# Kernel optimization log

Hardware: AMD Instinct MI355X
Metric: run time of the kernel (lower is better)

Reference implementation:

```python
import jax, jax.numpy as jnp
import numpy as np

N, E, B = 10000, 160000, 64
ND, ED, H, L, C = 128, 64, 256, 4, 10
LN_EPS = 1e-5


def _layernorm(x, g, b):
    mu = jnp.mean(x, axis=-1, keepdims=True)
    var = jnp.mean(jnp.square(x - mu), axis=-1, keepdims=True)
    return (x - mu) * jax.lax.rsqrt(var + LN_EPS) * g + b


def setup_inputs() -> dict:
    key = jax.random.key(0)
    ks = jax.random.split(key, 24)

    def w(k, shape, fan_in):
        return jax.random.normal(k, shape, jnp.float32) * (1.0 / np.sqrt(fan_in))

    node_features = jax.random.normal(ks[0], (N, ND), jnp.float32)
    edge_index = jax.random.randint(ks[1], (2, E), 0, N, jnp.int64)
    edge_features = jax.random.normal(ks[2], (E, ED), jnp.float32)
    # deterministic sorted batch assignment (no empty graphs)
    batch = (jnp.arange(N, dtype=jnp.int64) * B) // N

    inp = dict(
        node_features=node_features,
        edge_index=edge_index,
        edge_features=edge_features,
        batch=batch,
        node_W=w(ks[3], (ND, H), ND), node_b=jnp.zeros((H,), jnp.float32),
        edge_W=w(ks[4], (ED, H), ED), edge_b=jnp.zeros((H,), jnp.float32),
        msg_W1=w(ks[5], (L, 3 * H, H), 3 * H), msg_b1=jnp.zeros((L, H), jnp.float32),
        msg_W2=w(ks[6], (L, H, H), H), msg_b2=jnp.zeros((L, H), jnp.float32),
        upd_W1=w(ks[7], (L, 2 * H, H), 2 * H), upd_b1=jnp.zeros((L, H), jnp.float32),
        upd_W2=w(ks[8], (L, H, H), H), upd_b2=jnp.zeros((L, H), jnp.float32),
        ln_g=jnp.ones((L, H), jnp.float32), ln_b=jnp.zeros((L, H), jnp.float32),
        ro_W1=w(ks[9], (H, H), H), ro_b1=jnp.zeros((H,), jnp.float32),
        ro_W2=w(ks[10], (H, C), H), ro_b2=jnp.zeros((C,), jnp.float32),
    )
    return inp


def _forward(node_features, edge_features, node_W, node_b, edge_W, edge_b,
             msg_W1, msg_b1, msg_W2, msg_b2, upd_W1, upd_b1, upd_W2, upd_b2,
             ln_g, ln_b, ro_W1, ro_b1, ro_W2, ro_b2, edge_index, batch):
    src, dst = edge_index[0], edge_index[1]
    x = node_features @ node_W + node_b            # [N, H]
    edge_attr = edge_features @ edge_W + edge_b    # [E, H]
    for l in range(L):
        # batched gather-MLP over all edges (vectorized version of the per-edge loop)
        m_in = jnp.concatenate([x[src], x[dst], edge_attr], axis=-1)  # [E, 3H]
        msg = jax.nn.relu(m_in @ msg_W1[l] + msg_b1[l]) @ msg_W2[l] + msg_b2[l]
        agg = jnp.zeros_like(x).at[dst].add(msg)    # scatter-add by destination
        u_in = jnp.concatenate([x, agg], axis=-1)   # [N, 2H]
        upd = jax.nn.relu(u_in @ upd_W1[l] + upd_b1[l]) @ upd_W2[l] + upd_b2[l]
        x = _layernorm(x + upd, ln_g[l], ln_b[l])
    # global mean pool per graph
    sums = jax.ops.segment_sum(x, batch, num_segments=B)
    cnts = jax.ops.segment_sum(jnp.ones((x.shape[0], 1), x.dtype), batch, num_segments=B)
    pooled = sums / cnts                            # [B, H]
    return jax.nn.relu(pooled @ ro_W1 + ro_b1) @ ro_W2 + ro_b2  # [B, C]


def reference(node_features, edge_index, edge_features, batch,
              node_W, node_b, edge_W, edge_b,
              msg_W1, msg_b1, msg_W2, msg_b2,
              upd_W1, upd_b1, upd_W2, upd_b2,
              ln_g, ln_b, ro_W1, ro_b1, ro_W2, ro_b2):
    return _forward(node_features, edge_features, node_W, node_b, edge_W, edge_b,
                    msg_W1, msg_b1, msg_W2, msg_b2, upd_W1, upd_b1, upd_W2, upd_b2,
                    ln_g, ln_b, ro_W1, ro_b1, ro_W2, ro_b2, edge_index, batch)
```

## Files before the change

### kernel.cpp

```cpp
#include <hip/hip_runtime.h>
#include <cstdint>
#include <cstddef>


typedef unsigned short u16;
typedef __attribute__((ext_vector_type(4))) float f32x4;
typedef __attribute__((ext_vector_type(8))) short bf16x8;
typedef __attribute__((ext_vector_type(4))) short s16x4;

constexpr int kN  = 10000;
constexpr int kE  = 160000;
constexpr int kB  = 64;
constexpr int kH  = 256;
constexpr int kL  = 4;
constexpr int kC  = 10;
constexpr float kEps = 1e-5f;

struct __align__(16) F4 { float v[4]; };
__device__ __forceinline__ F4 ldF4(const float* p) { return *reinterpret_cast<const F4*>(p); }

__device__ __forceinline__ u16 f2bf(float f) {
    unsigned u = __builtin_bit_cast(unsigned, f);
    return (u16)((u + 0x7fffu + ((u >> 16) & 1u)) >> 16);
}
__device__ __forceinline__ float bf2f(u16 h) {
    return __builtin_bit_cast(float, (unsigned)h << 16);
}
__device__ __forceinline__ unsigned cvtpk(float lo, float hi) {
    unsigned r;
    asm("v_cvt_pk_bf16_f32 %0, %1, %2" : "=v"(r) : "v"(lo), "v"(hi));
    return r;
}

typedef __attribute__((address_space(1))) void GV;
typedef __attribute__((address_space(3))) void LV;
__device__ __forceinline__ void gl_lds16(const void* g, void* l) {
    __builtin_amdgcn_global_load_lds((GV*)g, (LV*)l, 16, 0, 0);
}
__device__ __forceinline__ void dma_w16k(const u16* __restrict__ Wc, char* lds, int tid) {
    const int w = tid >> 6, lane = tid & 63;
    char* lb = lds + w * 4096;
    const char* gb = (const char*)Wc + w * 4096 + lane * 16;
    #pragma unroll
    for (int i = 0; i < 4; ++i) gl_lds16(gb + i * 1024, lb + i * 1024);
}

__global__ void k_detect_i64(const unsigned* __restrict__ w, int* __restrict__ flag) {
    if (threadIdx.x == 0 && blockIdx.x == 0) {
        int is64 = 1;
        for (int i = 0; i < 64; ++i)
            if (w[2*i + 1] != 0u) { is64 = 0; break; }
        *flag = is64;
    }
}
__global__ void k_cvt_idx(const unsigned* __restrict__ w, const int* __restrict__ flag,
                          int* __restrict__ out, int n) {
    int i = blockIdx.x * 256 + threadIdx.x;
    if (i < n) out[i] = (*flag) ? (int)w[2*i] : (int)w[i];
}

__global__ __launch_bounds__(256) void k_hist(const int* __restrict__ dst,
                                              int* __restrict__ cnt) {
    int e = blockIdx.x * 256 + threadIdx.x;
    if (e < kE) atomicAdd(&cnt[dst[e]], 1);
}
__global__ __launch_bounds__(256) void k_scan(const int* __restrict__ cnt,
                                              int* __restrict__ cur) {
    __shared__ int part[256];
    const int t = threadIdx.x;
    const int per = (kN + 255) / 256;
    int s = 0;
    for (int i = 0; i < per; ++i) {
        int idx = t * per + i;
        if (idx < kN) s += cnt[idx];
    }
    int own = s;
    part[t] = s; __syncthreads();
    for (int off = 1; off < 256; off <<= 1) {
        int v = (t >= off) ? part[t - off] : 0;
        __syncthreads();
        part[t] += v;
        __syncthreads();
    }
    int run = part[t] - own;
    for (int i = 0; i < per; ++i) {
        int idx = t * per + i;
        if (idx < kN) { cur[idx] = run; run += cnt[idx]; }
    }
}
__global__ __launch_bounds__(256) void k_scatter(
    const int* __restrict__ src, const int* __restrict__ dst,
    int* __restrict__ cur, int* __restrict__ perm,
    int* __restrict__ ssorted, int* __restrict__ dsorted) {
    int e = blockIdx.x * 256 + threadIdx.x;
    if (e < kE) {
        int d = dst[e];
        int p = atomicAdd(&cur[d], 1);
        perm[p] = e;
        ssorted[p] = src[e];
        dsorted[p] = d;
    }
}

__global__ __launch_bounds__(256) void k_prep_w(
    const float* __restrict__ mW1, const float* __restrict__ mW2,
    const float* __restrict__ uW1, const float* __restrict__ uW2,
    u16* __restrict__ tm1, u16* __restrict__ tm2,
    u16* __restrict__ tu1, u16* __restrict__ tu2)
{
    int idx = blockIdx.x * 256 + threadIdx.x;
    const int S1 = kL * 768 * 256;
    const int S2 = S1 + kL * 256 * 256;
    const int S3 = S2 + kL * 512 * 256;
    const int S4 = S3 + kL * 256 * 256;
    const float* src; u16* dst; int K, r;
    if (idx < S1)      { src = mW1; dst = tm1; K = 768; r = idx; }
    else if (idx < S2) { src = mW2; dst = tm2; K = 256; r = idx - S1; }
    else if (idx < S3) { src = uW1; dst = tu1; K = 512; r = idx - S2; }
    else if (idx < S4) { src = uW2; dst = tu2; K = 256; r = idx - S3; }
    else return;
    int per = K * 256;
    int layer = r / per, rr = r - layer * per;
    int k = rr >> 8, n = rr & 255;
    int kc = k >> 5, kg = (k >> 3) & 3, e = k & 7;
    dst[(size_t)layer * per + (size_t)kc * 8192 + n * 32 + ((kg ^ ((n >> 1) & 3)) << 3) + e]
        = f2bf(src[(size_t)layer * per + rr]);
}

__global__ __launch_bounds__(256) void k_prep_ef(
    const float* __restrict__ ef, const int* __restrict__ perm,
    u16* __restrict__ efs)
{
    int idx = blockIdx.x * 256 + threadIdx.x;
    if (idx >= kE * 64) return;
    int p = idx >> 6, k = idx & 63;
    float v = ef[(size_t)perm[p] * 64 + k];
    int row = p & 63, blk = p >> 6;
    int kc = k >> 5, kg = (k >> 3) & 3, e = k & 7;
    efs[(size_t)blk * 4096 + kc * 2048 + row * 32
        + ((kg ^ ((row >> 1) & 3)) << 3) + e] = f2bf(v);
}

__global__ __launch_bounds__(256) void k_prep_m(
    const float* __restrict__ eW, const float* __restrict__ eb,
    const float* __restrict__ mW1, const float* __restrict__ mb1,
    u16* __restrict__ tmc, float* __restrict__ b1p)
{
    __shared__ float sWe[16 * 256];
    const int l = blockIdx.x, rq = blockIdx.y, t = threadIdx.x;
    const int r0 = rq * 16;
    #pragma unroll
    for (int i = 0; i < 16; ++i) sWe[i * 256 + t] = eW[(size_t)(r0 + i) * 256 + t];
    __syncthreads();
    const float* W1c = mW1 + (size_t)l * 768 * 256 + (size_t)512 * 256;
    float m[16];
    #pragma unroll
    for (int r = 0; r < 16; ++r) m[r] = 0.f;
    float bp = (rq == 0) ? mb1[l * 256 + t] : 0.f;
    for (int j = 0; j < 256; ++j) {
        float wv = W1c[(size_t)j * 256 + t];
        if (rq == 0) bp = fmaf(eb[j], wv, bp);
        #pragma unroll
        for (int r = 0; r < 16; ++r) m[r] = fmaf(sWe[r * 256 + j], wv, m[r]);
    }
    if (rq == 0) b1p[l * 256 + t] = bp;
    #pragma unroll
    for (int r = 0; r < 16; ++r) {
        int k = r0 + r;
        int kc = k >> 5, kg = (k >> 3) & 3, e = k & 7;
        tmc[(size_t)l * 16384 + (size_t)kc * 8192 + t * 32
            + ((kg ^ ((t >> 1) & 3)) << 3) + e] = f2bf(m[r]);
    }
}

__global__ __launch_bounds__(256) void k_encode_nodes(
    const float* __restrict__ nf, const float* __restrict__ W,
    const float* __restrict__ b, float* __restrict__ x, u16* __restrict__ x_bf)
{
    __shared__ float s_nf[4 * 128];
    const int n0 = blockIdx.x * 4;
    const int tid = threadIdx.x;
    reinterpret_cast<float2*>(s_nf)[tid] =
        reinterpret_cast<const float2*>(nf + (size_t)n0 * 128)[tid];
    __syncthreads();
    float acc[4] = {0.f, 0.f, 0.f, 0.f};
    for (int k = 0; k < 128; ++k) {
        float w = W[k * kH + tid];
        #pragma unroll
        for (int r = 0; r < 4; ++r) acc[r] = fmaf(s_nf[r * 128 + k], w, acc[r]);
    }
    float bias = b[tid];
    #pragma unroll
    for (int r = 0; r < 4; ++r) {
        float o = acc[r] + bias;
        x[(size_t)(n0 + r) * kH + tid] = o;
        x_bf[(size_t)(n0 + r) * kH + tid] = f2bf(o);
    }
}

__device__ __forceinline__ bf16x8 rdfrag(const char* lds, int n, int kg) {
    return *reinterpret_cast<const bf16x8*>(lds + n * 64 + ((kg ^ ((n >> 1) & 3)) << 4));
}
__device__ __forceinline__ bf16x8 rdH(const char* H, int row, int kbyte) {
    return *reinterpret_cast<const bf16x8*>(H + row * 512 + (kbyte ^ ((row & 7) << 4)));
}

__global__ __launch_bounds__(256, 3) void k_node_pre(
    const u16* __restrict__ x_bf, const u16* __restrict__ Wt1,
    u16* __restrict__ y_a, u16* __restrict__ y_b)
{
    __shared__ char sWt[16384];
    __shared__ char sA[4096];
    const int tid = threadIdx.x;
    const int n0 = blockIdx.x * 64;
    const int half = blockIdx.y;
    const u16* Wt = Wt1 + (size_t)half * 8 * 8192;
    u16* y = half ? y_b : y_a;
    const int w = tid >> 6, lane = tid & 63;
    const int lr = lane & 15, lg = lane >> 4;
    const int srow = tid >> 2, skg = tid & 3;
    const int kg_src = skg ^ ((srow >> 1) & 3);
    int gnode = n0 + srow; if (gnode >= kN) gnode = kN - 1;

    f32x4 acc[4][4];
    #pragma unroll
    for (int i = 0; i < 4; ++i)
        #pragma unroll
        for (int j = 0; j < 4; ++j) acc[i][j] = (f32x4){0.f, 0.f, 0.f, 0.f};

    for (int kc = 0; kc < 8; ++kc) {
        __syncthreads();
        dma_w16k(Wt + (size_t)kc * 8192, sWt, tid);
        gl_lds16(x_bf + (size_t)gnode * kH + kc * 32 + kg_src * 8, sA + w * 1024);
        __syncthreads();
        bf16x8 af[4], bfm[4];
        #pragma unroll
        for (int i = 0; i < 4; ++i) af[i] = rdfrag(sWt, w * 64 + i * 16 + lr, lg);
        #pragma unroll
        for (int j = 0; j < 4; ++j) bfm[j] = rdfrag(sA, j * 16 + lr, lg);
        #pragma unroll
        for (int i = 0; i < 4; ++i)
            #pragma unroll
            for (int j = 0; j < 4; ++j)
                acc[i][j] = __builtin_amdgcn_mfma_f32_16x16x32_bf16(af[i], bfm[j], acc[i][j], 0, 0, 0);
    }
    #pragma unroll
    for (int i = 0; i < 4; ++i) {
        const int hc0 = w * 64 + i * 16 + lg * 4;
        #pragma unroll
        for (int j = 0; j < 4; ++j) {
            const int node = n0 + j * 16 + lr;
            if (node < kN) {
                uint2 o;
                o.x = cvtpk(acc[i][j][0], acc[i][j][1]);
                o.y = cvtpk(acc[i][j][2], acc[i][j][3]);
                *reinterpret_cast<uint2*>(y + (size_t)node * kH + hc0) = o;
            }
        }
    }
}

__global__ __launch_bounds__(256, 3) void k_msg(
    const u16* __restrict__ efs,
    const int* __restrict__ ssorted, const int* __restrict__ dsorted,
    const u16* __restrict__ y_a, const u16* __restrict__ y_b,
    const u16* __restrict__ Wtm, const float* __restrict__ b1p,
    const u16* __restrict__ Wt2, const float* __restrict__ b2,
    float* __restrict__ agg)
{
    __shared__ char sWt[16384];
    __shared__ char sA[4096];
    __shared__ char sH[32768];
    __shared__ int sDst[64];

    const int tid = threadIdx.x;
    const int nwg = gridDim.x;
    const int q8 = nwg >> 3, r8 = nwg & 7;
    const int xcd = blockIdx.x & 7, sub = blockIdx.x >> 3;
    const int bid = (xcd < r8 ? xcd * (q8 + 1) : r8 * (q8 + 1) + (xcd - r8) * q8) + sub;
    const int e0 = bid * 64;

    const int w = tid >> 6, lane = tid & 63;
    const int lr = lane & 15, lg = lane >> 4;

    if (tid < 64) sDst[tid] = dsorted[e0 + tid];
    int esrc[4], edst[4];
    #pragma unroll
    for (int j = 0; j < 4; ++j) {
        esrc[j] = ssorted[e0 + j * 16 + lr];
        edst[j] = dsorted[e0 + j * 16 + lr];
    }

    f32x4 acc[4][4];
    #pragma unroll
    for (int i = 0; i < 4; ++i)
        #pragma unroll
        for (int j = 0; j < 4; ++j) acc[i][j] = (f32x4){0.f, 0.f, 0.f, 0.f};

    for (int kc = 0; kc < 2; ++kc) {
        __syncthreads();
        dma_w16k(Wtm + (size_t)kc * 8192, sWt, tid);
        gl_lds16((const char*)efs + (size_t)bid * 8192 + kc * 4096 + w * 1024 + lane * 16,
                 sA + w * 1024);
        __syncthreads();
        bf16x8 af[4], bfm[4];
        #pragma unroll
        for (int i = 0; i < 4; ++i) af[i] = rdfrag(sWt, w * 64 + i * 16 + lr, lg);
        #pragma unroll
        for (int j = 0; j < 4; ++j) bfm[j] = rdfrag(sA, j * 16 + lr, lg);
        #pragma unroll
        for (int i = 0; i < 4; ++i)
            #pragma unroll
            for (int j = 0; j < 4; ++j)
                acc[i][j] = __builtin_amdgcn_mfma_f32_16x16x32_bf16(af[i], bfm[j], acc[i][j], 0, 0, 0);
    }

    #pragma unroll
    for (int j = 0; j < 4; ++j) {
        const int edge = j * 16 + lr;
        const u16* pa = y_a + (size_t)esrc[j] * kH;
        const u16* pb = y_b + (size_t)edst[j] * kH;
        uint2 ya[4], yb[4];
        #pragma unroll
        for (int i = 0; i < 4; ++i) {
            const int hc0 = w * 64 + i * 16 + lg * 4;
            ya[i] = *reinterpret_cast<const uint2*>(pa + hc0);
            yb[i] = *reinterpret_cast<const uint2*>(pb + hc0);
        }
        #pragma unroll
        for (int i = 0; i < 4; ++i) {
            const int hc0 = w * 64 + i * 16 + lg * 4;
            const F4 bb = ldF4(b1p + hc0);
            float s0 = __builtin_bit_cast(float, ya[i].x << 16) + __builtin_bit_cast(float, yb[i].x << 16);
            float s1 = __builtin_bit_cast(float, ya[i].x & 0xffff0000u) + __builtin_bit_cast(float, yb[i].x & 0xffff0000u);
            float s2 = __builtin_bit_cast(float, ya[i].y << 16) + __builtin_bit_cast(float, yb[i].y << 16);
            float s3 = __builtin_bit_cast(float, ya[i].y & 0xffff0000u) + __builtin_bit_cast(float, yb[i].y & 0xffff0000u);
            float h0 = acc[i][j][0] + bb.v[0] + s0; h0 = h0 > 0.f ? h0 : 0.f;
            float h1 = acc[i][j][1] + bb.v[1] + s1; h1 = h1 > 0.f ? h1 : 0.f;
            float h2 = acc[i][j][2] + bb.v[2] + s2; h2 = h2 > 0.f ? h2 : 0.f;
            float h3 = acc[i][j][3] + bb.v[3] + s3; h3 = h3 > 0.f ? h3 : 0.f;
            uint2 o; o.x = cvtpk(h0, h1); o.y = cvtpk(h2, h3);
            int byte = edge * 512 + hc0 * 2;
            *reinterpret_cast<uint2*>(sH + (byte ^ ((edge & 7) << 4))) = o;
            acc[i][j] = (f32x4){0.f, 0.f, 0.f, 0.f};
        }
    }
    __syncthreads();

    for (int kc = 0; kc < 8; ++kc) {
        __syncthreads();
        dma_w16k(Wt2 + (size_t)kc * 8192, sWt, tid);
        __syncthreads();
        bf16x8 af2[4], bf2[4];
        #pragma unroll
        for (int i = 0; i < 4; ++i) af2[i] = rdH(sH, i * 16 + lr, kc * 64 + lg * 16);
        #pragma unroll
        for (int j = 0; j < 4; ++j) bf2[j] = rdfrag(sWt, w * 64 + j * 16 + lr, lg);
        #pragma unroll
        for (int i = 0; i < 4; ++i)
            #pragma unroll
            for (int j = 0; j < 4; ++j)
                acc[i][j] = __builtin_amdgcn_mfma_f32_16x16x32_bf16(af2[i], bf2[j], acc[i][j], 0, 0, 0);
    }

    __syncthreads();
    #pragma unroll
    for (int j = 0; j < 4; ++j) {
        const int oc = w * 64 + j * 16 + lr;
        const float b2v = b2[oc];
        #pragma unroll
        for (int i = 0; i < 4; ++i) {
            unsigned p01 = cvtpk(acc[i][j][0] + b2v, acc[i][j][1] + b2v);
            unsigned p23 = cvtpk(acc[i][j][2] + b2v, acc[i][j][3] + b2v);
            int eb0 = i * 16 + lg * 4;
            *reinterpret_cast<u16*>(sH + (((eb0 + 0) * 512 + oc * 2) ^ (((eb0 + 0) & 7) << 4))) = (u16)p01;
            *reinterpret_cast<u16*>(sH + (((eb0 + 1) * 512 + oc * 2) ^ (((eb0 + 1) & 7) << 4))) = (u16)(p01 >> 16);
            *reinterpret_cast<u16*>(sH + (((eb0 + 2) * 512 + oc * 2) ^ (((eb0 + 2) & 7) << 4))) = (u16)p23;
            *reinterpret_cast<u16*>(sH + (((eb0 + 3) * 512 + oc * 2) ^ (((eb0 + 3) & 7) << 4))) = (u16)(p23 >> 16);
        }
    }
    __syncthreads();

    {
        const int col = tid;
        float run = 0.f;
        int prev = sDst[0];
        #pragma unroll 1
        for (int eb = 0; eb < 8; ++eb) {
            float vv[8]; int dd[8];
            #pragma unroll
            for (int t = 0; t < 8; ++t) {
                int e = eb * 8 + t;
                int byte = e * 512 + col * 2;
                vv[t] = bf2f(*reinterpret_cast<const u16*>(sH + (byte ^ ((e & 7) << 4))));
                dd[t] = sDst[e];
            }
            #pragma unroll
            for (int t = 0; t < 8; ++t) {
                if (dd[t] != prev) {
                    unsafeAtomicAdd(agg + (size_t)prev * kH + col, run);
                    run = 0.f; prev = dd[t];
                }
                run += vv[t];
            }
        }
        unsafeAtomicAdd(agg + (size_t)prev * kH + col, run);
    }
}

__global__ __launch_bounds__(256, 2) void k_upd(
    float* __restrict__ x, u16* __restrict__ x_bf,
    float* __restrict__ agg,
    const u16* __restrict__ Wt1, const float* __restrict__ b1,
    const u16* __restrict__ Wt2, const float* __restrict__ b2,
    const float* __restrict__ lng, const float* __restrict__ lnb,
    const u16* __restrict__ Wt1n, int do_y,
    u16* __restrict__ y_a, u16* __restrict__ y_b)
{
    __shared__ char sWt[2][16384];
    __shared__ char sA[2][4096];
    __shared__ char sH[32768];

    const int tid = threadIdx.x;
    const int n0 = blockIdx.x * 64;
    const int w = tid >> 6, lane = tid & 63;
    const int lr = lane & 15, lg = lane >> 4;
    const int srow = tid >> 2, skg = tid & 3;
    const int kg_src = skg ^ ((srow >> 1) & 3);
    int gnode = n0 + srow; if (gnode >= kN) gnode = kN - 1;

    dma_w16k(Wt1, sWt[0], tid);
    gl_lds16(x_bf + (size_t)gnode * kH + kg_src * 8, sA[0] + w * 1024);

    f32x4 acc[4][4];
    #pragma unroll
    for (int i = 0; i < 4; ++i)
        #pragma unroll
        for (int j = 0; j < 4; ++j) acc[i][j] = (f32x4){0.f, 0.f, 0.f, 0.f};
    __syncthreads();

    for (int kc = 0; kc < 16; ++kc) {
        const int cur = kc & 1, nxt = cur ^ 1;
        bool do_agg = false; F4 a0, a1;
        if (kc < 15) {
            dma_w16k(Wt1 + (size_t)(kc + 1) * 8192, sWt[nxt], tid);
            if (kc + 1 < 8) {
                gl_lds16(x_bf + (size_t)gnode * kH + (kc + 1) * 32 + kg_src * 8,
                         sA[nxt] + w * 1024);
            } else {
                const float* ap = agg + (size_t)gnode * kH + (kc + 1 - 8) * 32 + skg * 8;
                a0 = ldF4(ap); a1 = ldF4(ap + 4); do_agg = true;
            }
        } else {
            dma_w16k(Wt2, sWt[nxt], tid);
        }
        bf16x8 af[4], bfm[4];
        #pragma unroll
        for (int i = 0; i < 4; ++i) af[i] = rdfrag(sWt[cur], w * 64 + i * 16 + lr, lg);
        #pragma unroll
        for (int j = 0; j < 4; ++j) bfm[j] = rdfrag(sA[cur], j * 16 + lr, lg);
        #pragma unroll
        for (int i = 0; i < 4; ++i)
            #pragma unroll
            for (int j = 0; j < 4; ++j)
                acc[i][j] = __builtin_amdgcn_mfma_f32_16x16x32_bf16(af[i], bfm[j], acc[i][j], 0, 0, 0);
        if (do_agg) {
            int4 bv;
            bv.x = (int)cvtpk(a0.v[0], a0.v[1]);
            bv.y = (int)cvtpk(a0.v[2], a0.v[3]);
            bv.z = (int)cvtpk(a1.v[0], a1.v[1]);
            bv.w = (int)cvtpk(a1.v[2], a1.v[3]);
            *reinterpret_cast<int4*>(sA[nxt] + srow * 64 + ((skg ^ ((srow >> 1) & 3)) << 4)) = bv;
        }
        __syncthreads();
    }

    #pragma unroll
    for (int i = 0; i < 4; ++i) {
        const int hc0 = w * 64 + i * 16 + lg * 4;
        const F4 bb = ldF4(b1 + hc0);
        #pragma unroll
        for (int j = 0; j < 4; ++j) {
            const int row = j * 16 + lr;
            float h0 = acc[i][j][0] + bb.v[0]; h0 = h0 > 0.f ? h0 : 0.f;
            float h1 = acc[i][j][1] + bb.v[1]; h1 = h1 > 0.f ? h1 : 0.f;
            float h2 = acc[i][j][2] + bb.v[2]; h2 = h2 > 0.f ? h2 : 0.f;
            float h3 = acc[i][j][3] + bb.v[3]; h3 = h3 > 0.f ? h3 : 0.f;
            uint2 o; o.x = cvtpk(h0, h1); o.y = cvtpk(h2, h3);
            int byte = row * 512 + hc0 * 2;
            *reinterpret_cast<uint2*>(sH + (byte ^ ((row & 7) << 4))) = o;
            acc[i][j] = (f32x4){0.f, 0.f, 0.f, 0.f};
        }
    }
    __syncthreads();

    {
        float4 z = make_float4(0.f, 0.f, 0.f, 0.f);
        float4* bp = reinterpret_cast<float4*>(agg + (size_t)n0 * kH);
        #pragma unroll
        for (int i = 0; i < 16; ++i) {
            int idx = i * 256 + tid;
            int row = idx >> 6;
            if (n0 + row < kN) bp[idx] = z;
        }
    }

    for (int kc = 0; kc < 8; ++kc) {
        const int cur = kc & 1, nxt = cur ^ 1;
        if (kc < 7) dma_w16k(Wt2 + (size_t)(kc + 1) * 8192, sWt[nxt], tid);
        bf16x8 af2[4], bf2[4];
        #pragma unroll
        for (int i = 0; i < 4; ++i) af2[i] = rdH(sH, i * 16 + lr, kc * 64 + lg * 16);
        #pragma unroll
        for (int j = 0; j < 4; ++j) bf2[j] = rdfrag(sWt[cur], w * 64 + j * 16 + lr, lg);
        #pragma unroll
        for (int i = 0; i < 4; ++i)
            #pragma unroll
            for (int j = 0; j < 4; ++j)
                acc[i][j] = __builtin_amdgcn_mfma_f32_16x16x32_bf16(af2[i], bf2[j], acc[i][j], 0, 0, 0);
        __syncthreads();
    }

    float b2v[4], gv[4], bvn[4];
    #pragma unroll
    for (int j = 0; j < 4; ++j) {
        int oc = w * 64 + j * 16 + lr;
        b2v[j] = b2[oc]; gv[j] = lng[oc]; bvn[j] = lnb[oc];
    }
    #pragma unroll
    for (int i = 0; i < 4; ++i)
        #pragma unroll
        for (int j = 0; j < 4; ++j) {
            int oc = w * 64 + j * 16 + lr;
            #pragma unroll
            for (int q = 0; q < 4; ++q) {
                int node = n0 + i * 16 + lg * 4 + q;
                int ncl = node < kN ? node : kN - 1;
                acc[i][j][q] += b2v[j] + x[(size_t)ncl * kH + oc];
            }
        }

    float (*red)[64][2] = reinterpret_cast<float(*)[64][2]>(sA[0]);
    float2* mstd = reinterpret_cast<float2*>(sA[0] + 2048);
    __syncthreads();
    #pragma unroll
    for (int i = 0; i < 4; ++i)
        #pragma unroll
        for (int q = 0; q < 4; ++q) {
            float s = acc[i][0][q] + acc[i][1][q] + acc[i][2][q] + acc[i][3][q];
            float ss = acc[i][0][q] * acc[i][0][q] + acc[i][1][q] * acc[i][1][q]
                     + acc[i][2][q] * acc[i][2][q] + acc[i][3][q] * acc[i][3][q];
            #pragma unroll
            for (int m = 1; m < 16; m <<= 1) { s += __shfl_xor(s, m); ss += __shfl_xor(ss, m); }
            if (lr == 0) { red[w][i * 16 + lg * 4 + q][0] = s; red[w][i * 16 + lg * 4 + q][1] = ss; }
        }
    __syncthreads();
    if (tid < 64) {
        float s = red[0][tid][0] + red[1][tid][0] + red[2][tid][0] + red[3][tid][0];
        float ss = red[0][tid][1] + red[1][tid][1] + red[2][tid][1] + red[3][tid][1];
        float mean = s * (1.f / 256.f);
        float var = ss * (1.f / 256.f) - mean * mean;
        mstd[tid] = make_float2(mean, rsqrtf(var + kEps));
    }
    __syncthreads();
    #pragma unroll
    for (int i = 0; i < 4; ++i)
        #pragma unroll
        for (int j = 0; j < 4; ++j) {
            int oc = w * 64 + j * 16 + lr;
            #pragma unroll
            for (int q = 0; q < 4; ++q) {
                int nn = i * 16 + lg * 4 + q;
                int node = n0 + nn;
                if (node < kN) {
                    float2 ms = mstd[nn];
                    float o = (acc[i][j][q] - ms.x) * ms.y * gv[j] + bvn[j];
                    u16 ob = f2bf(o);
                    x[(size_t)node * kH + oc] = o;
                    x_bf[(size_t)node * kH + oc] = ob;
                    if (do_y) {
                        int byte = nn * 512 + oc * 2;
                        *reinterpret_cast<u16*>(sH + (byte ^ ((nn & 7) << 4))) = ob;
                    }
                }
            }
        }

    if (do_y) {
        __syncthreads();
        dma_w16k(Wt1n, sWt[0], tid);
        #pragma unroll
        for (int i = 0; i < 4; ++i)
            #pragma unroll
            for (int j = 0; j < 4; ++j) acc[i][j] = (f32x4){0.f, 0.f, 0.f, 0.f};
        __syncthreads();
        for (int c = 0; c < 16; ++c) {
            const int cur = c & 1;
            if (c < 15) dma_w16k(Wt1n + (size_t)(c + 1) * 8192, sWt[cur ^ 1], tid);
            bf16x8 af[4], bfm[4];
            #pragma unroll
            for (int i = 0; i < 4; ++i) af[i] = rdfrag(sWt[cur], w * 64 + i * 16 + lr, lg);
            #pragma unroll
            for (int j = 0; j < 4; ++j) bfm[j] = rdH(sH, j * 16 + lr, (c & 7) * 64 + lg * 16);
            #pragma unroll
            for (int i = 0; i < 4; ++i)
                #pragma unroll
                for (int j = 0; j < 4; ++j)
                    acc[i][j] = __builtin_amdgcn_mfma_f32_16x16x32_bf16(af[i], bfm[j], acc[i][j], 0, 0, 0);
            if (c == 7 || c == 15) {
                u16* y = (c == 7) ? y_a : y_b;
                #pragma unroll
                for (int i = 0; i < 4; ++i) {
                    const int hc0 = w * 64 + i * 16 + lg * 4;
                    #pragma unroll
                    for (int j = 0; j < 4; ++j) {
                        const int node = n0 + j * 16 + lr;
                        if (node < kN) {
                            uint2 o;
                            o.x = cvtpk(acc[i][j][0], acc[i][j][1]);
                            o.y = cvtpk(acc[i][j][2], acc[i][j][3]);
                            *reinterpret_cast<uint2*>(y + (size_t)node * kH + hc0) = o;
                        }
                        acc[i][j] = (f32x4){0.f, 0.f, 0.f, 0.f};
                    }
                }
            }
            __syncthreads();
        }
    }
}

__device__ __forceinline__ int lower_bound_i(const int* a, int n, int v) {
    int lo = 0, hi = n;
    while (lo < hi) { int m = (lo + hi) >> 1; if (a[m] < v) lo = m + 1; else hi = m; }
    return lo;
}

__global__ __launch_bounds__(256) void k_pool_ro(
    const float* __restrict__ x, const int* __restrict__ batch,
    const float* __restrict__ W1, const float* __restrict__ b1,
    const float* __restrict__ W2, const float* __restrict__ b2,
    float* __restrict__ out)
{
    __shared__ float ph[kH];
    __shared__ float h1[kH];
    const int b = blockIdx.x, t = threadIdx.x;
    const int s = lower_bound_i(batch, kN, b);
    const int e = lower_bound_i(batch, kN, b + 1);
    float acc = 0.f;
    for (int i = s; i < e; ++i) acc += x[(size_t)i * kH + t];
    ph[t] = acc / (float)(e - s);
    __syncthreads();
    float a = b1[t];
    for (int k = 0; k < kH; ++k) a = fmaf(ph[k], W1[k * kH + t], a);
    h1[t] = a > 0.f ? a : 0.f;
    __syncthreads();
    if (t < kC) {
        float o = b2[t];
        for (int k = 0; k < kH; ++k) o = fmaf(h1[k], W2[k * kC + t], o);
        out[b * kC + t] = o;
    }
}

extern "C" void kernel_launch(void* const* d_in, const int* in_sizes, int n_in,
                              void* d_out, int out_size, void* d_ws, size_t ws_size,
                              hipStream_t stream)
{
    const float* nf     = (const float*)d_in[0];
    const void*  ei_raw = d_in[1];
    const float* ef     = (const float*)d_in[2];
    const void*  ba_raw = d_in[3];
    const float* node_W = (const float*)d_in[4];
    const float* node_b = (const float*)d_in[5];
    const float* edge_W = (const float*)d_in[6];
    const float* edge_b = (const float*)d_in[7];
    const float* msg_W1 = (const float*)d_in[8];
    const float* msg_b1 = (const float*)d_in[9];
    const float* msg_W2 = (const float*)d_in[10];
    const float* msg_b2 = (const float*)d_in[11];
    const float* upd_W1 = (const float*)d_in[12];
    const float* upd_b1 = (const float*)d_in[13];
    const float* upd_W2 = (const float*)d_in[14];
    const float* upd_b2 = (const float*)d_in[15];
    const float* ln_g   = (const float*)d_in[16];
    const float* ln_b   = (const float*)d_in[17];
    const float* ro_W1  = (const float*)d_in[18];
    const float* ro_b1  = (const float*)d_in[19];
    const float* ro_W2  = (const float*)d_in[20];
    const float* ro_b2  = (const float*)d_in[21];

    char* p = (char*)d_ws;
    auto alloc = [&](size_t bytes) { char* r = p; p += (bytes + 255) & ~(size_t)255; return r; };
    float* x    = (float*)alloc((size_t)kN * kH * 4);
    float* agg  = (float*)alloc((size_t)kN * kH * 4);
    u16* x_bf   = (u16*)alloc((size_t)kN * kH * 2);
    u16* y_a    = (u16*)alloc((size_t)kN * kH * 2);
    u16* y_b    = (u16*)alloc((size_t)kN * kH * 2);
    u16* efs    = (u16*)alloc((size_t)kE * 64 * 2);
    u16* tm1 = (u16*)alloc((size_t)kL * 768 * 256 * 2);
    u16* tm2 = (u16*)alloc((size_t)kL * 256 * 256 * 2);
    u16* tu1 = (u16*)alloc((size_t)kL * 512 * 256 * 2);
    u16* tu2 = (u16*)alloc((size_t)kL * 256 * 256 * 2);
    u16* tmc = (u16*)alloc((size_t)kL * 64 * 256 * 2);
    float* b1p = (float*)alloc((size_t)kL * 256 * 4);
    int* ei32 = (int*)alloc((size_t)2 * kE * 4);
    int* ba32 = (int*)alloc((size_t)kN * 4);
    int* cnt  = (int*)alloc((size_t)kN * 4);
    int* cur  = (int*)alloc((size_t)kN * 4);
    int* perm = (int*)alloc((size_t)kE * 4);
    int* ssorted = (int*)alloc((size_t)kE * 4);
    int* dsorted = (int*)alloc((size_t)kE * 4);
    int* flag = (int*)alloc(4);

    k_detect_i64<<<1, 64, 0, stream>>>((const unsigned*)ei_raw, flag);
    k_cvt_idx<<<(2 * kE + 255) / 256, 256, 0, stream>>>((const unsigned*)ei_raw, flag, ei32, 2 * kE);
    k_cvt_idx<<<(kN + 255) / 256, 256, 0, stream>>>((const unsigned*)ba_raw, flag, ba32, kN);
    const int* src = ei32;
    const int* dst = ei32 + kE;

    hipMemsetAsync(cnt, 0, (size_t)kN * 4, stream);
    k_hist<<<(kE + 255) / 256, 256, 0, stream>>>(dst, cnt);
    k_scan<<<1, 256, 0, stream>>>(cnt, cur);
    k_scatter<<<(kE + 255) / 256, 256, 0, stream>>>(src, dst, cur, perm, ssorted, dsorted);

    const int prep_elems = kL * (768 + 256 + 512 + 256) * 256;
    k_prep_w<<<(prep_elems + 255) / 256, 256, 0, stream>>>(
        msg_W1, msg_W2, upd_W1, upd_W2, tm1, tm2, tu1, tu2);
    k_prep_m<<<dim3(kL, 4), 256, 0, stream>>>(edge_W, edge_b, msg_W1, msg_b1, tmc, b1p);
    k_prep_ef<<<(kE * 64 + 255) / 256, 256, 0, stream>>>(ef, perm, efs);

    k_encode_nodes<<<kN / 4, 256, 0, stream>>>(nf, node_W, node_b, x, x_bf);

    hipMemsetAsync(agg, 0, (size_t)kN * kH * sizeof(float), stream);
    k_node_pre<<<dim3((kN + 63) / 64, 2), 256, 0, stream>>>(x_bf, tm1, y_a, y_b);

    for (int l = 0; l < kL; ++l) {
        k_msg<<<kE / 64, 256, 0, stream>>>(efs, ssorted, dsorted, y_a, y_b,
            tmc + (size_t)l * 64 * 256, b1p + l * 256,
            tm2 + (size_t)l * 256 * 256, msg_b2 + l * kH, agg);
        const int do_y = (l < kL - 1) ? 1 : 0;
        k_upd<<<(kN + 63) / 64, 256, 0, stream>>>(x, x_bf, agg,
            tu1 + (size_t)l * 512 * 256, upd_b1 + l * kH,
            tu2 + (size_t)l * 256 * 256, upd_b2 + l * kH,
            ln_g + l * kH, ln_b + l * kH,
            tm1 + (size_t)(l + 1 < kL ? l + 1 : 0) * 768 * 256, do_y, y_a, y_b);
    }

    k_pool_ro<<<kB, 256, 0, stream>>>(x, ba32, ro_W1, ro_b1, ro_W2, ro_b2, (float*)d_out);
}
```

Before: 658.6 us.

## Load MFMA operands directly from global memory and unfuse next-layer node projection

Replaces the LDS staging of weight and activation fragments (global_load_lds plus barriers) in k_node_pre, k_msg and k_upd with direct per-lane global vector loads, relying on L1/L2 caches for reuse. k_msg now prefetches the gathered y_a/y_b rows before the edge-feature GEMM. The next-layer node projection is no longer fused into k_upd; k_node_pre runs separately for each layer. The aim is to cut LDS traffic, barriers and occupancy limits, at the cost of redundant global/cache loads and an extra launch per layer.

```diff
diff --git a/kernel.cpp b/kernel.cpp
--- a/kernel.cpp
+++ b/kernel.cpp
@@ -32,17 +32,8 @@
     return r;
 }
 
-typedef __attribute__((address_space(1))) void GV;
-typedef __attribute__((address_space(3))) void LV;
-__device__ __forceinline__ void gl_lds16(const void* g, void* l) {
-    __builtin_amdgcn_global_load_lds((GV*)g, (LV*)l, 16, 0, 0);
-}
-__device__ __forceinline__ void dma_w16k(const u16* __restrict__ Wc, char* lds, int tid) {
-    const int w = tid >> 6, lane = tid & 63;
-    char* lb = lds + w * 4096;
-    const char* gb = (const char*)Wc + w * 4096 + lane * 16;
-    #pragma unroll
-    for (int i = 0; i < 4; ++i) gl_lds16(gb + i * 1024, lb + i * 1024);
+__device__ __forceinline__ bf16x8 g_frag(const u16* __restrict__ g, int n, int kg) {
+    return *reinterpret_cast<const bf16x8*>(g + n * 32 + ((kg ^ ((n >> 1) & 3)) << 3));
 }
 
 __global__ void k_detect_i64(const unsigned* __restrict__ w, int* __restrict__ flag) {
@@ -198,19 +189,14 @@
     }
 }
 
-__device__ __forceinline__ bf16x8 rdfrag(const char* lds, int n, int kg) {
-    return *reinterpret_cast<const bf16x8*>(lds + n * 64 + ((kg ^ ((n >> 1) & 3)) << 4));
-}
 __device__ __forceinline__ bf16x8 rdH(const char* H, int row, int kbyte) {
     return *reinterpret_cast<const bf16x8*>(H + row * 512 + (kbyte ^ ((row & 7) << 4)));
 }
 
-__global__ __launch_bounds__(256, 3) void k_node_pre(
+__global__ __launch_bounds__(256) void k_node_pre(
     const u16* __restrict__ x_bf, const u16* __restrict__ Wt1,
     u16* __restrict__ y_a, u16* __restrict__ y_b)
 {
-    __shared__ char sWt[16384];
-    __shared__ char sA[4096];
     const int tid = threadIdx.x;
     const int n0 = blockIdx.x * 64;
     const int half = blockIdx.y;
@@ -218,9 +204,13 @@
     u16* y = half ? y_b : y_a;
     const int w = tid >> 6, lane = tid & 63;
     const int lr = lane & 15, lg = lane >> 4;
-    const int srow = tid >> 2, skg = tid & 3;
-    const int kg_src = skg ^ ((srow >> 1) & 3);
-    int gnode = n0 + srow; if (gnode >= kN) gnode = kN - 1;
+
+    int nd[4];
+    #pragma unroll
+    for (int j = 0; j < 4; ++j) {
+        int n = n0 + j * 16 + lr;
+        nd[j] = n < kN ? n : kN - 1;
+    }
 
     f32x4 acc[4][4];
     #pragma unroll
@@ -228,16 +218,15 @@
         #pragma unroll
         for (int j = 0; j < 4; ++j) acc[i][j] = (f32x4){0.f, 0.f, 0.f, 0.f};
 
+    #pragma unroll 2
     for (int kc = 0; kc < 8; ++kc) {
-        __syncthreads();
-        dma_w16k(Wt + (size_t)kc * 8192, sWt, tid);
-        gl_lds16(x_bf + (size_t)gnode * kH + kc * 32 + kg_src * 8, sA + w * 1024);
-        __syncthreads();
         bf16x8 af[4], bfm[4];
         #pragma unroll
-        for (int i = 0; i < 4; ++i) af[i] = rdfrag(sWt, w * 64 + i * 16 + lr, lg);
-        #pragma unroll
-        for (int j = 0; j < 4; ++j) bfm[j] = rdfrag(sA, j * 16 + lr, lg);
+        for (int i = 0; i < 4; ++i) af[i] = g_frag(Wt + kc * 8192, w * 64 + i * 16 + lr, lg);
+        #pragma unroll
+        for (int j = 0; j < 4; ++j)
+            bfm[j] = *reinterpret_cast<const bf16x8*>(
+                x_bf + (size_t)nd[j] * kH + kc * 32 + lg * 8);
         #pragma unroll
         for (int i = 0; i < 4; ++i)
             #pragma unroll
@@ -268,8 +257,6 @@
     const u16* __restrict__ Wt2, const float* __restrict__ b2,
     float* __restrict__ agg)
 {
-    __shared__ char sWt[16384];
-    __shared__ char sA[4096];
     __shared__ char sH[32768];
     __shared__ int sDst[64];
 
@@ -284,11 +271,20 @@
     const int lr = lane & 15, lg = lane >> 4;
 
     if (tid < 64) sDst[tid] = dsorted[e0 + tid];
-    int esrc[4], edst[4];
+
+    uint2 ya[4][4], yb[4][4];
     #pragma unroll
     for (int j = 0; j < 4; ++j) {
-        esrc[j] = ssorted[e0 + j * 16 + lr];
-        edst[j] = dsorted[e0 + j * 16 + lr];
+        const int es = ssorted[e0 + j * 16 + lr];
+        const int ed = dsorted[e0 + j * 16 + lr];
+        const u16* pa = y_a + (size_t)es * kH;
+        const u16* pb = y_b + (size_t)ed * kH;
+        #pragma unroll
+        for (int i = 0; i < 4; ++i) {
+            const int hc0 = w * 64 + i * 16 + lg * 4;
+            ya[j][i] = *reinterpret_cast<const uint2*>(pa + hc0);
+            yb[j][i] = *reinterpret_cast<const uint2*>(pb + hc0);
+        }
     }
 
     f32x4 acc[4][4];
@@ -297,17 +293,18 @@
         #pragma unroll
         for (int j = 0; j < 4; ++j) acc[i][j] = (f32x4){0.f, 0.f, 0.f, 0.f};
 
+    #pragma unroll
     for (int kc = 0; kc < 2; ++kc) {
-        __syncthreads();
-        dma_w16k(Wtm + (size_t)kc * 8192, sWt, tid);
-        gl_lds16((const char*)efs + (size_t)bid * 8192 + kc * 4096 + w * 1024 + lane * 16,
-                 sA + w * 1024);
-        __syncthreads();
+        const u16* efc = efs + (size_t)bid * 4096 + kc * 2048;
         bf16x8 af[4], bfm[4];
         #pragma unroll
-        for (int i = 0; i < 4; ++i) af[i] = rdfrag(sWt, w * 64 + i * 16 + lr, lg);
-        #pragma unroll
-        for (int j = 0; j < 4; ++j) bfm[j] = rdfrag(sA, j * 16 + lr, lg);
+        for (int i = 0; i < 4; ++i) af[i] = g_frag(Wtm + kc * 8192, w * 64 + i * 16 + lr, lg);
+        #pragma unroll
+        for (int j = 0; j < 4; ++j) {
+            int row = j * 16 + lr;
+            bfm[j] = *reinterpret_cast<const bf16x8*>(
+                efc + row * 32 + ((lg ^ ((row >> 1) & 3)) << 3));
+        }
         #pragma unroll
         for (int i = 0; i < 4; ++i)
             #pragma unroll
@@ -318,23 +315,14 @@
     #pragma unroll
     for (int j = 0; j < 4; ++j) {
         const int edge = j * 16 + lr;
-        const u16* pa = y_a + (size_t)esrc[j] * kH;
-        const u16* pb = y_b + (size_t)edst[j] * kH;
-        uint2 ya[4], yb[4];
-        #pragma unroll
-        for (int i = 0; i < 4; ++i) {
-            const int hc0 = w * 64 + i * 16 + lg * 4;
-            ya[i] = *reinterpret_cast<const uint2*>(pa + hc0);
-            yb[i] = *reinterpret_cast<const uint2*>(pb + hc0);
-        }
         #pragma unroll
         for (int i = 0; i < 4; ++i) {
             const int hc0 = w * 64 + i * 16 + lg * 4;
             const F4 bb = ldF4(b1p + hc0);
-            float s0 = __builtin_bit_cast(float, ya[i].x << 16) + __builtin_bit_cast(float, yb[i].x << 16);
-            float s1 = __builtin_bit_cast(float, ya[i].x & 0xffff0000u) + __builtin_bit_cast(float, yb[i].x & 0xffff0000u);
-            float s2 = __builtin_bit_cast(float, ya[i].y << 16) + __builtin_bit_cast(float, yb[i].y << 16);
-            float s3 = __builtin_bit_cast(float, ya[i].y & 0xffff0000u) + __builtin_bit_cast(float, yb[i].y & 0xffff0000u);
+            float s0 = __builtin_bit_cast(float, ya[j][i].x << 16) + __builtin_bit_cast(float, yb[j][i].x << 16);
+            float s1 = __builtin_bit_cast(float, ya[j][i].x & 0xffff0000u) + __builtin_bit_cast(float, yb[j][i].x & 0xffff0000u);
+            float s2 = __builtin_bit_cast(float, ya[j][i].y << 16) + __builtin_bit_cast(float, yb[j][i].y << 16);
+            float s3 = __builtin_bit_cast(float, ya[j][i].y & 0xffff0000u) + __builtin_bit_cast(float, yb[j][i].y & 0xffff0000u);
             float h0 = acc[i][j][0] + bb.v[0] + s0; h0 = h0 > 0.f ? h0 : 0.f;
             float h1 = acc[i][j][1] + bb.v[1] + s1; h1 = h1 > 0.f ? h1 : 0.f;
             float h2 = acc[i][j][2] + bb.v[2] + s2; h2 = h2 > 0.f ? h2 : 0.f;
@@ -347,15 +335,13 @@
     }
     __syncthreads();
 
+    #pragma unroll 2
     for (int kc = 0; kc < 8; ++kc) {
-        __syncthreads();
-        dma_w16k(Wt2 + (size_t)kc * 8192, sWt, tid);
-        __syncthreads();
         bf16x8 af2[4], bf2[4];
         #pragma unroll
         for (int i = 0; i < 4; ++i) af2[i] = rdH(sH, i * 16 + lr, kc * 64 + lg * 16);
         #pragma unroll
-        for (int j = 0; j < 4; ++j) bf2[j] = rdfrag(sWt, w * 64 + j * 16 + lr, lg);
+        for (int j = 0; j < 4; ++j) bf2[j] = g_frag(Wt2 + kc * 8192, w * 64 + j * 16 + lr, lg);
         #pragma unroll
         for (int i = 0; i < 4; ++i)
             #pragma unroll
@@ -408,71 +394,71 @@
     }
 }
 
-__global__ __launch_bounds__(256, 2) void k_upd(
+__global__ __launch_bounds__(256) void k_upd(
     float* __restrict__ x, u16* __restrict__ x_bf,
     float* __restrict__ agg,
     const u16* __restrict__ Wt1, const float* __restrict__ b1,
     const u16* __restrict__ Wt2, const float* __restrict__ b2,
-    const float* __restrict__ lng, const float* __restrict__ lnb,
-    const u16* __restrict__ Wt1n, int do_y,
-    u16* __restrict__ y_a, u16* __restrict__ y_b)
-{
-    __shared__ char sWt[2][16384];
-    __shared__ char sA[2][4096];
+    const float* __restrict__ lng, const float* __restrict__ lnb)
+{
     __shared__ char sH[32768];
+    __shared__ float red[4][64][2];
+    __shared__ float2 mstd[64];
 
     const int tid = threadIdx.x;
     const int n0 = blockIdx.x * 64;
     const int w = tid >> 6, lane = tid & 63;
     const int lr = lane & 15, lg = lane >> 4;
-    const int srow = tid >> 2, skg = tid & 3;
-    const int kg_src = skg ^ ((srow >> 1) & 3);
-    int gnode = n0 + srow; if (gnode >= kN) gnode = kN - 1;
-
-    dma_w16k(Wt1, sWt[0], tid);
-    gl_lds16(x_bf + (size_t)gnode * kH + kg_src * 8, sA[0] + w * 1024);
+
+    int nd[4];
+    #pragma unroll
+    for (int j = 0; j < 4; ++j) {
+        int n = n0 + j * 16 + lr;
+        nd[j] = n < kN ? n : kN - 1;
+    }
 
     f32x4 acc[4][4];
     #pragma unroll
     for (int i = 0; i < 4; ++i)
         #pragma unroll
         for (int j = 0; j < 4; ++j) acc[i][j] = (f32x4){0.f, 0.f, 0.f, 0.f};
-    __syncthreads();
-
-    for (int kc = 0; kc < 16; ++kc) {
-        const int cur = kc & 1, nxt = cur ^ 1;
-        bool do_agg = false; F4 a0, a1;
-        if (kc < 15) {
-            dma_w16k(Wt1 + (size_t)(kc + 1) * 8192, sWt[nxt], tid);
-            if (kc + 1 < 8) {
-                gl_lds16(x_bf + (size_t)gnode * kH + (kc + 1) * 32 + kg_src * 8,
-                         sA[nxt] + w * 1024);
-            } else {
-                const float* ap = agg + (size_t)gnode * kH + (kc + 1 - 8) * 32 + skg * 8;
-                a0 = ldF4(ap); a1 = ldF4(ap + 4); do_agg = true;
-            }
-        } else {
-            dma_w16k(Wt2, sWt[nxt], tid);
-        }
+
+    #pragma unroll 2
+    for (int kc = 0; kc < 8; ++kc) {
         bf16x8 af[4], bfm[4];
         #pragma unroll
-        for (int i = 0; i < 4; ++i) af[i] = rdfrag(sWt[cur], w * 64 + i * 16 + lr, lg);
-        #pragma unroll
-        for (int j = 0; j < 4; ++j) bfm[j] = rdfrag(sA[cur], j * 16 + lr, lg);
+        for (int i = 0; i < 4; ++i) af[i] = g_frag(Wt1 + kc * 8192, w * 64 + i * 16 + lr, lg);
+        #pragma unroll
+        for (int j = 0; j < 4; ++j)
+            bfm[j] = *reinterpret_cast<const bf16x8*>(
+                x_bf + (size_t)nd[j] * kH + kc * 32 + lg * 8);
         #pragma unroll
         for (int i = 0; i < 4; ++i)
             #pragma unroll
             for (int j = 0; j < 4; ++j)
                 acc[i][j] = __builtin_amdgcn_mfma_f32_16x16x32_bf16(af[i], bfm[j], acc[i][j], 0, 0, 0);
-        if (do_agg) {
-            int4 bv;
-            bv.x = (int)cvtpk(a0.v[0], a0.v[1]);
-            bv.y = (int)cvtpk(a0.v[2], a0.v[3]);
-            bv.z = (int)cvtpk(a1.v[0], a1.v[1]);
-            bv.w = (int)cvtpk(a1.v[2], a1.v[3]);
-            *reinterpret_cast<int4*>(sA[nxt] + srow * 64 + ((skg ^ ((srow >> 1) & 3)) << 4)) = bv;
-        }
-        __syncthreads();
+    }
+    #pragma unroll 2
+    for (int kc = 8; kc < 16; ++kc) {
+        bf16x8 af[4], bfm[4];
+        #pragma unroll
+        for (int i = 0; i < 4; ++i) af[i] = g_frag(Wt1 + kc * 8192, w * 64 + i * 16 + lr, lg);
+        #pragma unroll
+        for (int j = 0; j < 4; ++j) {
+            const float* ap = agg + (size_t)nd[j] * kH + (kc - 8) * 32 + lg * 8;
+            F4 a0 = ldF4(ap), a1 = ldF4(ap + 4);
+            uint4 u;
+            u.x = cvtpk(a0.v[0], a0.v[1]);
+            u.y = cvtpk(a0.v[2], a0.v[3]);
+            u.z = cvtpk(a1.v[0], a1.v[1]);
+            u.w = cvtpk(a1.v[2], a1.v[3]);
+            bfm[j] = __builtin_bit_cast(bf16x8, u);
+        }
+        #pragma unroll
+        for (int i = 0; i < 4; ++i)
+            #pragma unroll
+            for (int j = 0; j < 4; ++j)
+                acc[i][j] = __builtin_amdgcn_mfma_f32_16x16x32_bf16(af[i], bfm[j], acc[i][j], 0, 0, 0);
     }
 
     #pragma unroll
@@ -505,20 +491,18 @@
         }
     }
 
+    #pragma unroll 2
     for (int kc = 0; kc < 8; ++kc) {
-        const int cur = kc & 1, nxt = cur ^ 1;
-        if (kc < 7) dma_w16k(Wt2 + (size_t)(kc + 1) * 8192, sWt[nxt], tid);
         bf16x8 af2[4], bf2[4];
         #pragma unroll
         for (int i = 0; i < 4; ++i) af2[i] = rdH(sH, i * 16 + lr, kc * 64 + lg * 16);
         #pragma unroll
-        for (int j = 0; j < 4; ++j) bf2[j] = rdfrag(sWt[cur], w * 64 + j * 16 + lr, lg);
+        for (int j = 0; j < 4; ++j) bf2[j] = g_frag(Wt2 + kc * 8192, w * 64 + j * 16 + lr, lg);
         #pragma unroll
         for (int i = 0; i < 4; ++i)
             #pragma unroll
             for (int j = 0; j < 4; ++j)
                 acc[i][j] = __builtin_amdgcn_mfma_f32_16x16x32_bf16(af2[i], bf2[j], acc[i][j], 0, 0, 0);
-        __syncthreads();
     }
 
     float b2v[4], gv[4], bvn[4];
@@ -540,9 +524,6 @@
             }
         }
 
-    float (*red)[64][2] = reinterpret_cast<float(*)[64][2]>(sA[0]);
-    float2* mstd = reinterpret_cast<float2*>(sA[0] + 2048);
-    __syncthreads();
     #pragma unroll
     for (int i = 0; i < 4; ++i)
         #pragma unroll
@@ -575,59 +556,11 @@
                 if (node < kN) {
                     float2 ms = mstd[nn];
                     float o = (acc[i][j][q] - ms.x) * ms.y * gv[j] + bvn[j];
-                    u16 ob = f2bf(o);
                     x[(size_t)node * kH + oc] = o;
-                    x_bf[(size_t)node * kH + oc] = ob;
-                    if (do_y) {
-                        int byte = nn * 512 + oc * 2;
-                        *reinterpret_cast<u16*>(sH + (byte ^ ((nn & 7) << 4))) = ob;
-                    }
+                    x_bf[(size_t)node * kH + oc] = f2bf(o);
                 }
             }
         }
-
-    if (do_y) {
-        __syncthreads();
-        dma_w16k(Wt1n, sWt[0], tid);
-        #pragma unroll
-        for (int i = 0; i < 4; ++i)
-            #pragma unroll
-            for (int j = 0; j < 4; ++j) acc[i][j] = (f32x4){0.f, 0.f, 0.f, 0.f};
-        __syncthreads();
-        for (int c = 0; c < 16; ++c) {
-            const int cur = c & 1;
-            if (c < 15) dma_w16k(Wt1n + (size_t)(c + 1) * 8192, sWt[cur ^ 1], tid);
-            bf16x8 af[4], bfm[4];
-            #pragma unroll
-            for (int i = 0; i < 4; ++i) af[i] = rdfrag(sWt[cur], w * 64 + i * 16 + lr, lg);
-            #pragma unroll
-            for (int j = 0; j < 4; ++j) bfm[j] = rdH(sH, j * 16 + lr, (c & 7) * 64 + lg * 16);
-            #pragma unroll
-            for (int i = 0; i < 4; ++i)
-                #pragma unroll
-                for (int j = 0; j < 4; ++j)
-                    acc[i][j] = __builtin_amdgcn_mfma_f32_16x16x32_bf16(af[i], bfm[j], acc[i][j], 0, 0, 0);
-            if (c == 7 || c == 15) {
-                u16* y = (c == 7) ? y_a : y_b;
-                #pragma unroll
-                for (int i = 0; i < 4; ++i) {
-                    const int hc0 = w * 64 + i * 16 + lg * 4;
-                    #pragma unroll
-                    for (int j = 0; j < 4; ++j) {
-                        const int node = n0 + j * 16 + lr;
-                        if (node < kN) {
-                            uint2 o;
-                            o.x = cvtpk(acc[i][j][0], acc[i][j][1]);
-                            o.y = cvtpk(acc[i][j][2], acc[i][j][3]);
-                            *reinterpret_cast<uint2*>(y + (size_t)node * kH + hc0) = o;
-                        }
-                        acc[i][j] = (f32x4){0.f, 0.f, 0.f, 0.f};
-                    }
-                }
-            }
-            __syncthreads();
-        }
-    }
 }
 
 __device__ __forceinline__ int lower_bound_i(const int* a, int n, int v) {
@@ -730,20 +663,18 @@
     k_prep_ef<<<(kE * 64 + 255) / 256, 256, 0, stream>>>(ef, perm, efs);
 
     k_encode_nodes<<<kN / 4, 256, 0, stream>>>(nf, node_W, node_b, x, x_bf);
-
     hipMemsetAsync(agg, 0, (size_t)kN * kH * sizeof(float), stream);
-    k_node_pre<<<dim3((kN + 63) / 64, 2), 256, 0, stream>>>(x_bf, tm1, y_a, y_b);
 
     for (int l = 0; l < kL; ++l) {
+        k_node_pre<<<dim3((kN + 63) / 64, 2), 256, 0, stream>>>(
+            x_bf, tm1 + (size_t)l * 768 * 256, y_a, y_b);
         k_msg<<<kE / 64, 256, 0, stream>>>(efs, ssorted, dsorted, y_a, y_b,
             tmc + (size_t)l * 64 * 256, b1p + l * 256,
             tm2 + (size_t)l * 256 * 256, msg_b2 + l * kH, agg);
-        const int do_y = (l < kL - 1) ? 1 : 0;
         k_upd<<<(kN + 63) / 64, 256, 0, stream>>>(x, x_bf, agg,
             tu1 + (size_t)l * 512 * 256, upd_b1 + l * kH,
             tu2 + (size_t)l * 256 * 256, upd_b2 + l * kH,
-            ln_g + l * kH, ln_b + l * kH,
-            tm1 + (size_t)(l + 1 < kL ? l + 1 : 0) * 768 * 256, do_y, y_a, y_b);
+            ln_g + l * kH, ln_b + l * kH);
     }
 
     k_pool_ro<<<kB, 256, 0, stream>>>(x, ba32, ro_W1, ro_b1, ro_W2, ro_b2, (float*)d_out);
```

Measured after the change: 659.9 us. No clear change (+0.2%).
